# Kernel tuning notes

Measured on AMD Instinct MI355X. Metric: run time of the kernel, lower is better.

## Reference

```python
import jax, jax.numpy as jnp
import numpy as np

B, DIN, F, H, C = 8192, 2048, 2048, 2048, 345
EPS = 1e-5


def setup_inputs() -> dict:
    key = jax.random.key(0)
    ks = jax.random.split(key, 8)
    rng = np.random.default_rng(0)
    # labels and sort order (torch.sort is stable here via argsort kind='stable')
    y_np = rng.integers(0, C, size=B).astype(np.int64)
    order_np = np.argsort(y_np, kind='stable')
    ys = y_np[order_np]
    # per-class random permutations within each sorted segment (torch.randperm per interval)
    shuf1 = np.empty(B, dtype=np.int64)
    shuf2 = np.empty(B, dtype=np.int64)
    for c in np.unique(ys):
        idx = np.nonzero(ys == c)[0]
        shuf1[idx] = rng.permutation(idx)
        shuf2[idx] = rng.permutation(idx)
    s = 0.02  # weight init scale
    return {
        'x': jax.random.normal(ks[0], (B, DIN), jnp.float32),
        'lam': jnp.array([float(rng.beta(0.5, 0.5))], jnp.float32),
        'Wf': jax.random.normal(ks[1], (DIN, F), jnp.float32) * s,
        'bf': jnp.zeros((F,), jnp.float32),
        'W1': jax.random.normal(ks[2], (F, H), jnp.float32) * s,
        'b1': jnp.zeros((H,), jnp.float32),
        'g1': jnp.ones((H,), jnp.float32),
        'be1': jnp.zeros((H,), jnp.float32),
        'W2': jax.random.normal(ks[3], (H, H), jnp.float32) * s,
        'b2': jnp.zeros((H,), jnp.float32),
        'g2': jnp.ones((H,), jnp.float32),
        'be2': jnp.zeros((H,), jnp.float32),
        'W3': jax.random.normal(ks[4], (H, F), jnp.float32) * s,
        'b3': jnp.zeros((F,), jnp.float32),
        'g3': jnp.ones((F,), jnp.float32),
        'be3': jnp.zeros((F,), jnp.float32),
        'Wc': jax.random.normal(ks[5], (F, C), jnp.float32) * s,
        'bc': jnp.zeros((C,), jnp.float32),
        'y': jnp.asarray(y_np),
        'order': jnp.asarray(order_np),
        'shuf1': jnp.asarray(shuf1),
        'shuf2': jnp.asarray(shuf2),
    }


def _bn(x, g, b):
    # BatchNorm1d, training mode: biased batch stats
    m = jnp.mean(x, axis=0)
    v = jnp.var(x, axis=0)
    return (x - m) * jax.lax.rsqrt(v + EPS) * g + b


def reference(x, lam, Wf, bf, W1, b1, g1, be1, W2, b2, g2, be2, W3, b3, g3, be3, Wc, bc, y, order, shuf1, shuf2):
    lam = lam[0]
    xs = x[order]           # sorted-by-label gather (vectorized)
    ys = y[order]
    feat = jax.nn.relu(xs @ Wf + bf)                      # featurizer
    h = jax.nn.relu(_bn(feat @ W1 + b1, g1, be1))         # cdpl projector
    h = jax.nn.relu(_bn(h @ W2 + b2, g2, be2))
    proj = _bn(h @ W3 + b3, g3, be3)
    out = feat @ Wc + bc                                  # classifier logits
    out2, feat2 = out[shuf1], proj[shuf1]                 # per-class shuffles
    out3, feat3 = out[shuf2], proj[shuf2]
    out3 = lam * out2 + (1.0 - lam) * out3
    feat3 = lam * feat2 + (1.0 - lam) * feat3
    mse = lambda a, b: jnp.mean((a - b) ** 2)
    L_ind_logit = mse(out, out2)
    L_hdl_logit = mse(out, out3)
    L_ind_feat = 0.3 * mse(proj, feat2)
    L_hdl_feat = 0.3 * mse(proj, feat3)
    logp = jax.nn.log_softmax(out, axis=-1)
    cl_loss = -jnp.mean(jnp.take_along_axis(logp, ys[:, None], axis=-1))
    C_scale = jax.lax.stop_gradient(jnp.minimum(cl_loss, 1.0))  # .item() -> constant
    loss = cl_loss + C_scale * (lam * (L_ind_logit + L_ind_feat) + (1.0 - lam) * (L_hdl_logit + L_hdl_feat))
    return loss
```

## Files before the change

kernel.cpp:

```cpp
#include <hip/hip_runtime.h>

#define NB   8192
#define NF   2048
#define NC   345
#define NCP  384
#define EPSV 1e-5f

#define SX   (5.75f / 127.0f)
#define SW   (0.115f / 127.0f)
#define SF   (5.2f / 127.0f)
#define SH   (5.75f / 127.0f)
#define ST1  (3.34f / 127.0f)
#define ST2  (3.68f / 127.0f)
#define QX   (1.0f / SX)
#define QW   (1.0f / SW)
#define QF   (1.0f / SF)
#define QH   (1.0f / SH)
#define QT1  (1.0f / ST1)
#define QT2  (1.0f / ST2)

typedef __bf16 bf16x8 __attribute__((ext_vector_type(8)));
typedef float  f32x4  __attribute__((ext_vector_type(4)));
typedef int    i32x4  __attribute__((ext_vector_type(4)));

__device__ __forceinline__ float bs2f(unsigned int u) { return __uint_as_float(u << 16); }
__device__ __forceinline__ unsigned short f2bs(float f) {
    unsigned int u = __float_as_uint(f);
    u += 0x7fffu + ((u >> 16) & 1u);
    return (unsigned short)(u >> 16);
}
__device__ __forceinline__ int q8i(float v, float iq) {
    int t = __float2int_rn(v * iq);
    return t > 127 ? 127 : (t < -127 ? -127 : t);
}

#define GLD16(g, l)                                                                     \
    __builtin_amdgcn_global_load_lds((const __attribute__((address_space(1))) void*)(g),\
                                     (__attribute__((address_space(3))) void*)(l),      \
                                     16, 0, 0)

__global__ void k_gather(const float* __restrict__ x, const int* __restrict__ order,
                         char* __restrict__ xq) {
    const int row = blockIdx.x;
    const long src = order[row];
    const float4* xr = (const float4*)(x + src * 2048);
    float4 a = xr[threadIdx.x * 2 + 0];
    float4 b = xr[threadIdx.x * 2 + 1];
    unsigned int lo = (unsigned)(q8i(a.x, QX) & 255) | ((unsigned)(q8i(a.y, QX) & 255) << 8) |
                      ((unsigned)(q8i(a.z, QX) & 255) << 16) | ((unsigned)(q8i(a.w, QX) & 255) << 24);
    unsigned int hi = (unsigned)(q8i(b.x, QX) & 255) | ((unsigned)(q8i(b.y, QX) & 255) << 8) |
                      ((unsigned)(q8i(b.z, QX) & 255) << 16) | ((unsigned)(q8i(b.w, QX) & 255) << 24);
    uint2 o; o.x = lo; o.y = hi;
    ((uint2*)(xq + (long)row * 2048))[threadIdx.x] = o;
}

__global__ __launch_bounds__(256) void k_transpose4(
        const float* __restrict__ W0, const float* __restrict__ W1,
        const float* __restrict__ W2, const float* __restrict__ W3,
        char* __restrict__ Wt) {
    __shared__ float tile[32][133];
    const float* Wz = (blockIdx.z == 0) ? W0 : (blockIdx.z == 1) ? W1
                     : (blockIdx.z == 2) ? W2 : W3;
    char* out = Wt + (size_t)blockIdx.z * 2048 * 2048;
    const int n0 = blockIdx.x * 32, k0 = blockIdx.y * 128;
    const int t = threadIdx.x;
    #pragma unroll
    for (int i = 0; i < 16; i++) {
        const int e = t + i * 256;
        const int k = e >> 5, n = e & 31;
        tile[n][k] = Wz[(long)(k0 + k) * 2048 + n0 + n];
    }
    __syncthreads();
    #pragma unroll
    for (int i = 0; i < 4; i++) {
        const int e = t + i * 256;
        const int n = e >> 5;
        const int j = (e & 31) * 4;
        unsigned int o = (unsigned)(q8i(tile[n][j + 0], QW) & 255)
                       | ((unsigned)(q8i(tile[n][j + 1], QW) & 255) << 8)
                       | ((unsigned)(q8i(tile[n][j + 2], QW) & 255) << 16)
                       | ((unsigned)(q8i(tile[n][j + 3], QW) & 255) << 24);
        *(unsigned int*)&out[(long)(n0 + n) * 2048 + k0 + j] = o;
    }
}

__global__ void k_transposeC(const float* __restrict__ W, char* __restrict__ Wt8,
                             const float* __restrict__ bc, float* __restrict__ bcp,
                             int K, int N, int Npad) {
    __shared__ float tile[32][33];
    const int n0 = blockIdx.x * 32, k0 = blockIdx.y * 32;
    const int tx = threadIdx.x, ty = threadIdx.y;
    if (blockIdx.x == 0 && blockIdx.y == 0) {
        const int idx = ty * 32 + tx;
        for (int i = idx; i < Npad; i += 256) bcp[i] = (i < N) ? bc[i] : 0.f;
    }
    #pragma unroll
    for (int i = 0; i < 32; i += 8) {
        int n = n0 + tx, k = k0 + ty + i;
        tile[ty + i][tx] = (n < N) ? W[(long)k * N + n] : 0.f;
    }
    __syncthreads();
    #pragma unroll
    for (int i = 0; i < 32; i += 8) {
        int n = n0 + ty + i, k = k0 + tx;
        if (n < Npad) Wt8[(long)n * K + k] = (char)q8i(tile[tx][ty + i], QW);
    }
}

#define BARX  do { asm volatile("" ::: "memory"); __builtin_amdgcn_s_barrier(); \
                   asm volatile("" ::: "memory"); } while (0)
#define LGKM0 asm volatile("s_waitcnt lgkmcnt(0)" ::: "memory")
#define VMW4  asm volatile("s_waitcnt vmcnt(4)" ::: "memory")
#define VMW0  asm volatile("s_waitcnt vmcnt(0)" ::: "memory")

#define RDX(u, AV, BV) do {                                                            \
    const char* A_ = &L[((u) & 3) * 32768];                                            \
    const char* B_ = A_ + 16384;                                                       \
    _Pragma("unroll") for (int m_ = 0; m_ < 8; m_++)                                   \
        AV[m_] = *(const i32x4*)&A_[(wm * 128 + m_ * 16 + frow) * 64 + slt];           \
    _Pragma("unroll") for (int n_ = 0; n_ < 4; n_++)                                   \
        BV[n_] = *(const i32x4*)&B_[(wn * 64 + n_ * 16 + frow) * 64 + slt];            \
} while (0)

#define MMX(AV, BV) do {                                                               \
    __builtin_amdgcn_s_setprio(1);                                                     \
    _Pragma("unroll") for (int n_ = 0; n_ < 4; n_++)                                   \
    _Pragma("unroll") for (int m_ = 0; m_ < 8; m_++)                                   \
        acc[m_][n_] = __builtin_amdgcn_mfma_i32_16x16x64_i8(BV[n_], AV[m_],            \
                                                            acc[m_][n_], 0, 0, 0);    \
    __builtin_amdgcn_s_setprio(0);                                                     \
} while (0)

template <int RELU, int STATS>
__global__ __launch_bounds__(512, 2) void k_gemmq(
    const char* __restrict__ A,
    const char* __restrict__ Bt,
    const float* __restrict__ bias,
    char* __restrict__ C8,
    float* __restrict__ stats,
    float S, float IQ, int N, int K) {
    __shared__ char L[4 * 32768];
    const int tid  = threadIdx.x;
    const int lane = tid & 63;
    const int wv   = tid >> 6;
    const int frow = lane & 15;
    const int kg   = lane >> 4;
    const int wm   = wv >> 2;
    const int wn   = wv & 3;
    const int slt  = (kg ^ ((frow >> 1) & 3)) * 16;

    const int id  = blockIdx.x;
    const int xcd = id & 7, kid = id >> 3;
    const int brow = (xcd * 4 + (kid & 3)) * 256;
    const int bcol = (kid >> 2) * 256;

    const char* pA[2];
    const char* pB[2];
    #pragma unroll
    for (int i = 0; i < 2; i++) {
        const int q = tid + i * 512;
        const int j = q >> 2;
        const int c = (q & 3) ^ ((j >> 1) & 3);
        pA[i] = A  + (long)(brow + j) * K + c * 16;
        pB[i] = Bt + (long)(bcol + j) * K + c * 16;
    }

    i32x4 acc[8][4];
    #pragma unroll
    for (int m = 0; m < 8; m++)
        #pragma unroll
        for (int n = 0; n < 4; n++)
            #pragma unroll
            for (int r = 0; r < 4; r++) acc[m][n][r] = 0;

    auto stage = [&](int s) {
        char* Lb = &L[(s & 3) * 32768];
        const int ko = s * 64;
        GLD16(pA[0] + ko, Lb + wv * 1024);
        GLD16(pA[1] + ko, Lb + 8192 + wv * 1024);
        GLD16(pB[0] + ko, Lb + 16384 + wv * 1024);
        GLD16(pB[1] + ko, Lb + 24576 + wv * 1024);
    };

    i32x4 avA[8], bvA[4], avB[8], bvB[4];

    stage(0); stage(1); stage(2);
    VMW4; BARX;
    RDX(0, avA, bvA);

    for (int i = 0; i < 14; i++) {
        const int t = i * 2;
        RDX(t + 1, avB, bvB); stage(t + 3); MMX(avA, bvA); VMW4; BARX;
        RDX(t + 2, avA, bvA); stage(t + 4); MMX(avB, bvB); VMW4; BARX;
    }
    RDX(29, avB, bvB); stage(31); MMX(avA, bvA); VMW4; BARX;
    RDX(30, avA, bvA); MMX(avB, bvB); VMW0; BARX;
    RDX(31, avB, bvB); MMX(avA, bvA);
    MMX(avB, bvB);

    LGKM0; BARX;
    unsigned short* Ls = (unsigned short*)L;
    const int cbase = bcol + wn * 64 + kg * 4;
    #pragma unroll
    for (int n = 0; n < 4; n++) {
        const int col = cbase + n * 16;
        const float4 bb = *(const float4*)&bias[col];
        float s0_ = 0.f, s1_ = 0.f, s2_ = 0.f, s3_ = 0.f;
        float q0_ = 0.f, q1_ = 0.f, q2_ = 0.f, q3_ = 0.f;
        const int s8 = wn * 16 + n * 4 + kg;
        const int p8 = s8 ^ frow;
        #pragma unroll
        for (int m = 0; m < 8; m++) {
            const int rloc = wm * 128 + m * 16 + frow;
            float v0 = (float)acc[m][n][0] * S + bb.x;
            float v1 = (float)acc[m][n][1] * S + bb.y;
            float v2 = (float)acc[m][n][2] * S + bb.z;
            float v3 = (float)acc[m][n][3] * S + bb.w;
            if (STATS) { s0_ += v0; q0_ += v0 * v0; s1_ += v1; q1_ += v1 * v1;
                         s2_ += v2; q2_ += v2 * v2; s3_ += v3; q3_ += v3 * v3; }
            if (RELU) { v0 = fmaxf(v0, 0.f); v1 = fmaxf(v1, 0.f);
                        v2 = fmaxf(v2, 0.f); v3 = fmaxf(v3, 0.f); }
            ushort4 st; st.x = f2bs(v0); st.y = f2bs(v1); st.z = f2bs(v2); st.w = f2bs(v3);
            *(ushort4*)&Ls[rloc * 256 + p8 * 4] = st;
        }
        if (STATS) {
            #pragma unroll
            for (int off = 1; off <= 8; off <<= 1) {
                s0_ += __shfl_xor(s0_, off); s1_ += __shfl_xor(s1_, off);
                s2_ += __shfl_xor(s2_, off); s3_ += __shfl_xor(s3_, off);
                q0_ += __shfl_xor(q0_, off); q1_ += __shfl_xor(q1_, off);
                q2_ += __shfl_xor(q2_, off); q3_ += __shfl_xor(q3_, off);
            }
            if (frow == 0) {
                atomicAdd(&stats[col + 0], s0_); atomicAdd(&stats[col + 1], s1_);
                atomicAdd(&stats[col + 2], s2_); atomicAdd(&stats[col + 3], s3_);
                atomicAdd(&stats[N + col + 0], q0_); atomicAdd(&stats[N + col + 1], q1_);
                atomicAdd(&stats[N + col + 2], q2_); atomicAdd(&stats[N + col + 3], q3_);
            }
        }
    }
    LGKM0; BARX;
    #pragma unroll
    for (int it = 0; it < 16; it++) {
        const int c  = tid + it * 512;
        const int r  = c >> 5;
        const int a  = c & 31;
        const int x  = r & 15;
        const int a2 = a ^ (x >> 1);
        uint4 v = *(const uint4*)&Ls[r * 256 + a2 * 8];
        if (x & 1) { unsigned tx_ = v.x, ty_ = v.y; v.x = v.z; v.y = v.w; v.z = tx_; v.w = ty_; }
        const long grow = brow + r;
        const int  gcol = bcol + a * 8;
        unsigned int us[8] = {v.x & 0xffffu, v.x >> 16, v.y & 0xffffu, v.y >> 16,
                              v.z & 0xffffu, v.z >> 16, v.w & 0xffffu, v.w >> 16};
        unsigned int b[8];
        #pragma unroll
        for (int j = 0; j < 8; j++) b[j] = (unsigned)(q8i(bs2f(us[j]), IQ) & 255);
        uint2 o;
        o.x = b[0] | (b[1] << 8) | (b[2] << 16) | (b[3] << 24);
        o.y = b[4] | (b[5] << 8) | (b[6] << 16) | (b[7] << 24);
        *(uint2*)&C8[grow * N + gcol] = o;
    }
}

__global__ __launch_bounds__(256) void k_gemmc(const char* __restrict__ A,
                                               const char* __restrict__ Bt,
                                               const float* __restrict__ bias,
                                               unsigned short* __restrict__ outP,
                                               float S, int K) {
    __shared__ char As[2][8192];
    __shared__ char Bs[2][8192];
    const int tid  = threadIdx.x;
    const int lane = tid & 63;
    const int wv   = tid >> 6;
    const int brow = blockIdx.x * 128;
    const int bcol = blockIdx.y * 128;
    const int kz   = blockIdx.z;
    const long k0  = (long)kz * 1024;
    const int wr   = (wv >> 1) * 64;
    const int wc   = (wv & 1) * 64;
    const int frow = lane & 15;
    const int kg   = lane >> 4;
    const int slt  = (kg ^ ((frow >> 1) & 3)) * 16;

    const char* pA[2];
    const char* pB[2];
    #pragma unroll
    for (int i = 0; i < 2; i++) {
        const int q = tid + i * 256;
        const int j = q >> 2;
        const int c = (q & 3) ^ ((j >> 1) & 3);
        pA[i] = A  + (long)(brow + j) * K + k0 + c * 16;
        pB[i] = Bt + (long)(bcol + j) * K + k0 + c * 16;
    }

    i32x4 acc[4][4];
    #pragma unroll
    for (int m = 0; m < 4; m++)
        #pragma unroll
        for (int n = 0; n < 4; n++)
            #pragma unroll
            for (int r = 0; r < 4; r++) acc[m][n][r] = 0;

    auto stage = [&](int t, int b) {
        GLD16(pA[0] + t * 64, As[b] + wv * 1024);
        GLD16(pA[1] + t * 64, As[b] + 4096 + wv * 1024);
        GLD16(pB[0] + t * 64, Bs[b] + wv * 1024);
        GLD16(pB[1] + t * 64, Bs[b] + 4096 + wv * 1024);
    };

    stage(0, 0);
    __syncthreads();
    for (int t = 0; t < 16; t++) {
        if (t < 15) stage(t + 1, (t + 1) & 1);
        const int b = t & 1;
        i32x4 av[4], bv[4];
        #pragma unroll
        for (int m = 0; m < 4; m++)
            av[m] = *(const i32x4*)&As[b][(wr + m * 16 + frow) * 64 + slt];
        #pragma unroll
        for (int n = 0; n < 4; n++)
            bv[n] = *(const i32x4*)&Bs[b][(wc + n * 16 + frow) * 64 + slt];
        #pragma unroll
        for (int m = 0; m < 4; m++)
            #pragma unroll
            for (int n = 0; n < 4; n++)
                acc[m][n] = __builtin_amdgcn_mfma_i32_16x16x64_i8(bv[n], av[m],
                                                                  acc[m][n], 0, 0, 0);
        __syncthreads();
    }
    const int r0 = brow + wr + frow;
    const int c0 = bcol + wc + kg * 4;
    unsigned short* oz = outP + (long)kz * NB * NCP;
    #pragma unroll
    for (int n = 0; n < 4; n++) {
        const int col = c0 + n * 16;
        float4 bb = {0.f, 0.f, 0.f, 0.f};
        if (kz == 0) bb = *(const float4*)&bias[col];
        #pragma unroll
        for (int m = 0; m < 4; m++) {
            const long row = r0 + m * 16;
            ushort4 st;
            st.x = f2bs((float)acc[m][n][0] * S + bb.x);
            st.y = f2bs((float)acc[m][n][1] * S + bb.y);
            st.z = f2bs((float)acc[m][n][2] * S + bb.z);
            st.w = f2bs((float)acc[m][n][3] * S + bb.w);
            *(ushort4*)&oz[row * NCP + col] = st;
        }
    }
}

__global__ void k_bnapplyq8(const char* __restrict__ t8, const float* __restrict__ sums,
                            const float* __restrict__ g, const float* __restrict__ be,
                            char* __restrict__ o8, float St, int ncols) {
    const long i  = ((long)blockIdx.x * blockDim.x + threadIdx.x) * 8;
    const int  c0 = (int)(i & (ncols - 1));
    float sc[8], sh[8];
    #pragma unroll
    for (int j = 0; j < 8; j++) {
        const int c = c0 + j;
        const float m   = sums[c] * (1.f / NB);
        const float var = sums[ncols + c] * (1.f / NB) - m * m;
        const float s   = rsqrtf(var + EPSV) * g[c];
        sc[j] = s * St;
        sh[j] = be[c] - m * s;
    }
    uint2 v = *(const uint2*)(t8 + i);
    unsigned int b[8];
    #pragma unroll
    for (int j = 0; j < 8; j++) {
        const unsigned int w = (j < 4) ? v.x : v.y;
        const int raw = (int)(signed char)((w >> ((j & 3) * 8)) & 0xffu);
        float val = (float)raw * sc[j] + sh[j];
        val = fmaxf(val, 0.f);
        b[j] = (unsigned)(q8i(val, QH) & 255);
    }
    uint2 o;
    o.x = b[0] | (b[1] << 8) | (b[2] << 16) | (b[3] << 24);
    o.y = b[4] | (b[5] << 8) | (b[6] << 16) | (b[7] << 24);
    *(uint2*)(o8 + i) = o;
}

__global__ __launch_bounds__(256) void k_logitloss(const unsigned short* __restrict__ outP,
                            const int* __restrict__ y,
                            const int* __restrict__ order, const int* __restrict__ s1,
                            const int* __restrict__ s2, const float* __restrict__ lamp,
                            float* __restrict__ acc) {
    const int lane = threadIdx.x & 63;
    const int wv   = threadIdx.x >> 6;
    const int wid  = blockIdx.x * 4 + wv;
    const int nw   = gridDim.x * 4;
    const float lam = lamp[0];
    const unsigned short* P1 = outP + (long)NB * NCP;
    float ce = 0.f, d1 = 0.f, d2 = 0.f;
    for (int i = wid; i < NB; i += nw) {
        const long r0 = (long)i * NCP;
        const long r2 = (long)s1[i] * NCP;
        const long r3 = (long)s2[i] * NCP;
        float v[6];
        float mx = -1e30f;
        #pragma unroll
        for (int j = 0; j < 6; j++) {
            const int c = lane + j * 64;
            if (c < NC) {
                const float a  = bs2f(outP[r0 + c]) + bs2f(P1[r0 + c]);
                const float b  = bs2f(outP[r2 + c]) + bs2f(P1[r2 + c]);
                const float cc = bs2f(outP[r3 + c]) + bs2f(P1[r3 + c]);
                const float mix = lam * b + (1.f - lam) * cc;
                v[j] = a;
                d1 += (a - b) * (a - b);
                d2 += (a - mix) * (a - mix);
                mx = fmaxf(mx, a);
            } else v[j] = -1e30f;
        }
        #pragma unroll
        for (int off = 32; off; off >>= 1) mx = fmaxf(mx, __shfl_xor(mx, off));
        float se = 0.f;
        #pragma unroll
        for (int j = 0; j < 6; j++) se += expf(v[j] - mx);
        #pragma unroll
        for (int off = 32; off; off >>= 1) se += __shfl_xor(se, off);
        if (lane == 0) {
            const int yv = y[order[i]];
            const float oy = bs2f(outP[r0 + yv]) + bs2f(P1[r0 + yv]);
            ce += mx + logf(se) - oy;
        }
    }
    #pragma unroll
    for (int off = 32; off; off >>= 1) {
        d1 += __shfl_xor(d1, off);
        d2 += __shfl_xor(d2, off);
    }
    __shared__ float red[4][3];
    if (lane == 0) { red[wv][0] = ce; red[wv][1] = d1; red[wv][2] = d2; }
    __syncthreads();
    if (threadIdx.x == 0) {
        atomicAdd(&acc[0], red[0][0] + red[1][0] + red[2][0] + red[3][0]);
        atomicAdd(&acc[1], red[0][1] + red[1][1] + red[2][1] + red[3][1]);
        atomicAdd(&acc[2], red[0][2] + red[1][2] + red[2][2] + red[3][2]);
    }
}

__global__ __launch_bounds__(256) void k_featloss(const char* __restrict__ t3q,
                           const float* __restrict__ sums,
                           const float* __restrict__ g, const float* __restrict__ be,
                           const int* __restrict__ s1,
                           const int* __restrict__ s2, const float* __restrict__ lamp,
                           float* __restrict__ acc) {
    const int t = threadIdx.x;
    const float lam = lamp[0];
    float sc[8], sh[8];
    #pragma unroll
    for (int j = 0; j < 8; j++) {
        const int c = t * 8 + j;
        const float m   = sums[c] * (1.f / NB);
        const float var = sums[NF + c] * (1.f / NB) - m * m;
        const float s   = rsqrtf(var + EPSV) * g[c];
        sc[j] = s * ST2;
        sh[j] = be[c] - m * s;
    }
    float d1 = 0.f, d2 = 0.f;
    for (int i = blockIdx.x; i < NB; i += gridDim.x) {
        uint2 a = ((const uint2*)(t3q + (long)i * NF))[t];
        uint2 b = ((const uint2*)(t3q + (long)s1[i] * NF))[t];
        uint2 c = ((const uint2*)(t3q + (long)s2[i] * NF))[t];
        #pragma unroll
        for (int j = 0; j < 8; j++) {
            const unsigned int wa = (j < 4) ? a.x : a.y;
            const unsigned int wb = (j < 4) ? b.x : b.y;
            const unsigned int wc_ = (j < 4) ? c.x : c.y;
            const int sh8 = (j & 3) * 8;
            float pa = (float)(int)(signed char)((wa >> sh8) & 0xffu) * sc[j] + sh[j];
            float pb = (float)(int)(signed char)((wb >> sh8) & 0xffu) * sc[j] + sh[j];
            float pc = (float)(int)(signed char)((wc_ >> sh8) & 0xffu) * sc[j] + sh[j];
            float mix = lam * pb + (1.f - lam) * pc;
            d1 += (pa - pb) * (pa - pb);
            d2 += (pa - mix) * (pa - mix);
        }
    }
    #pragma unroll
    for (int off = 32; off; off >>= 1) {
        d1 += __shfl_xor(d1, off);
        d2 += __shfl_xor(d2, off);
    }
    __shared__ float r1[4], r2[4];
    if ((t & 63) == 0) { r1[t >> 6] = d1; r2[t >> 6] = d2; }
    __syncthreads();
    if (t == 0) {
        atomicAdd(&acc[3], r1[0] + r1[1] + r1[2] + r1[3]);
        atomicAdd(&acc[4], r2[0] + r2[1] + r2[2] + r2[3]);
    }
}

__global__ void k_final(const float* __restrict__ acc, const float* __restrict__ lamp,
                        float* __restrict__ outp) {
    const float lam = lamp[0];
    const float cl  = acc[0] * (1.f / NB);
    const float Lil = acc[1] * (1.f / ((float)NB * NC));
    const float Lhl = acc[2] * (1.f / ((float)NB * NC));
    const float Lif = 0.3f * acc[3] * (1.f / ((float)NB * NF));
    const float Lhf = 0.3f * acc[4] * (1.f / ((float)NB * NF));
    const float Cs  = fminf(cl, 1.f);
    outp[0] = cl + Cs * (lam * (Lil + Lif) + (1.f - lam) * (Lhl + Lhf));
}

extern "C" void kernel_launch(void* const* d_in, const int* in_sizes, int n_in,
                              void* d_out, int out_size, void* d_ws, size_t ws_size,
                              hipStream_t stream) {
    const float* x   = (const float*)d_in[0];
    const float* lam = (const float*)d_in[1];
    const float* Wf  = (const float*)d_in[2];
    const float* bf_ = (const float*)d_in[3];
    const float* W1  = (const float*)d_in[4];
    const float* b1  = (const float*)d_in[5];
    const float* g1  = (const float*)d_in[6];
    const float* be1 = (const float*)d_in[7];
    const float* W2  = (const float*)d_in[8];
    const float* b2  = (const float*)d_in[9];
    const float* g2  = (const float*)d_in[10];
    const float* be2 = (const float*)d_in[11];
    const float* W3  = (const float*)d_in[12];
    const float* b3  = (const float*)d_in[13];
    const float* g3  = (const float*)d_in[14];
    const float* be3 = (const float*)d_in[15];
    const float* Wc  = (const float*)d_in[16];
    const float* bc  = (const float*)d_in[17];
    const int* y     = (const int*)d_in[18];
    const int* order = (const int*)d_in[19];
    const int* s1    = (const int*)d_in[20];
    const int* s2    = (const int*)d_in[21];
    float* outp = (float*)d_out;

    char* ws = (char*)d_ws;
    const size_t MB = 1024 * 1024;
    char*  R0  = ws;
    char*  R2  = ws + 16 * MB;
    char*  R3  = ws + 32 * MB;
    unsigned short* outP = (unsigned short*)(ws + 48 * MB);
    char*  WT  = ws + 72 * MB;
    char*  WCT8 = ws + 88 * MB;
    float* stats = (float*)(ws + 89 * MB);
    float* accs  = stats + 3 * 4096;
    float* bcp   = accs + 16;

    hipMemsetAsync(stats, 0, (3 * 4096 + 8) * sizeof(float), stream);

    k_transpose4<<<dim3(64, 16, 4), 256, 0, stream>>>(Wf, W1, W2, W3, WT);
    k_transposeC<<<dim3(12, 64), dim3(32, 8), 0, stream>>>(Wc, WCT8, bc, bcp, 2048, NC, NCP);

    k_gather<<<NB, 256, 0, stream>>>(x, order, R0);

    k_gemmq<1, 0><<<256, 512, 0, stream>>>(R0, WT, bf_, R2, nullptr,
                                           SX * SW, QF, 2048, 2048);
    k_gemmc<<<dim3(64, 3, 2), 256, 0, stream>>>(R2, WCT8, bcp, outP, SF * SW, 2048);
    k_gemmq<0, 1><<<256, 512, 0, stream>>>(R2, WT + 4 * MB, b1, R3, stats,
                                           SF * SW, QT1, 2048, 2048);
    k_bnapplyq8<<<8192, 256, 0, stream>>>(R3, stats, g1, be1, R0, ST1, 2048);
    k_gemmq<0, 1><<<256, 512, 0, stream>>>(R0, WT + 8 * MB, b2, R3, stats + 4096,
                                           SH * SW, QT2, 2048, 2048);
    k_bnapplyq8<<<8192, 256, 0, stream>>>(R3, stats + 4096, g2, be2, R2, ST2, 2048);
    k_gemmq<0, 1><<<256, 512, 0, stream>>>(R2, WT + 12 * MB, b3, R3, stats + 8192,
                                           SH * SW, QT2, 2048, 2048);

    k_logitloss<<<512, 256, 0, stream>>>(outP, y, order, s1, s2, lam, accs);
    k_featloss<<<512, 256, 0, stream>>>(R3, stats + 8192, g3, be3, s1, s2, lam, accs);
    k_final<<<1, 1, 0, stream>>>(accs, lam, outp);
}
```

Baseline: 299.9 us.

## Merge independent kernels into combined launches to cut launch overhead

Three prep kernels (weight transposes, Wc transpose, input gather) become one launch whose work is chosen by block index. The classifier GEMM is moved later and co-launched with the first BN-apply, and the two loss kernels become one launch. The aim is fewer launches and more overlap of small independent work. The cost is mixed block types in one grid, which can change occupancy and scheduling. The classifier GEMM now also runs after the first projector GEMM instead of before it.

```diff
diff --git a/kernel.cpp b/kernel.cpp
--- a/kernel.cpp
+++ b/kernel.cpp
@@ -39,71 +39,70 @@
                                      (__attribute__((address_space(3))) void*)(l),      \
                                      16, 0, 0)
 
-__global__ void k_gather(const float* __restrict__ x, const int* __restrict__ order,
-                         char* __restrict__ xq) {
-    const int row = blockIdx.x;
-    const long src = order[row];
-    const float4* xr = (const float4*)(x + src * 2048);
-    float4 a = xr[threadIdx.x * 2 + 0];
-    float4 b = xr[threadIdx.x * 2 + 1];
-    unsigned int lo = (unsigned)(q8i(a.x, QX) & 255) | ((unsigned)(q8i(a.y, QX) & 255) << 8) |
-                      ((unsigned)(q8i(a.z, QX) & 255) << 16) | ((unsigned)(q8i(a.w, QX) & 255) << 24);
-    unsigned int hi = (unsigned)(q8i(b.x, QX) & 255) | ((unsigned)(q8i(b.y, QX) & 255) << 8) |
-                      ((unsigned)(q8i(b.z, QX) & 255) << 16) | ((unsigned)(q8i(b.w, QX) & 255) << 24);
-    uint2 o; o.x = lo; o.y = hi;
-    ((uint2*)(xq + (long)row * 2048))[threadIdx.x] = o;
-}
-
-__global__ __launch_bounds__(256) void k_transpose4(
+__global__ __launch_bounds__(256) void k_prep(
         const float* __restrict__ W0, const float* __restrict__ W1,
         const float* __restrict__ W2, const float* __restrict__ W3,
-        char* __restrict__ Wt) {
+        char* __restrict__ Wt,
+        const float* __restrict__ x, const int* __restrict__ order,
+        char* __restrict__ xq,
+        const float* __restrict__ Wc, char* __restrict__ WCT8,
+        const float* __restrict__ bc, float* __restrict__ bcp) {
     __shared__ float tile[32][133];
-    const float* Wz = (blockIdx.z == 0) ? W0 : (blockIdx.z == 1) ? W1
-                     : (blockIdx.z == 2) ? W2 : W3;
-    char* out = Wt + (size_t)blockIdx.z * 2048 * 2048;
-    const int n0 = blockIdx.x * 32, k0 = blockIdx.y * 128;
+    const int blk = blockIdx.x;
     const int t = threadIdx.x;
-    #pragma unroll
-    for (int i = 0; i < 16; i++) {
-        const int e = t + i * 256;
-        const int k = e >> 5, n = e & 31;
-        tile[n][k] = Wz[(long)(k0 + k) * 2048 + n0 + n];
-    }
-    __syncthreads();
-    #pragma unroll
-    for (int i = 0; i < 4; i++) {
-        const int e = t + i * 256;
-        const int n = e >> 5;
-        const int j = (e & 31) * 4;
-        unsigned int o = (unsigned)(q8i(tile[n][j + 0], QW) & 255)
-                       | ((unsigned)(q8i(tile[n][j + 1], QW) & 255) << 8)
-                       | ((unsigned)(q8i(tile[n][j + 2], QW) & 255) << 16)
-                       | ((unsigned)(q8i(tile[n][j + 3], QW) & 255) << 24);
-        *(unsigned int*)&out[(long)(n0 + n) * 2048 + k0 + j] = o;
-    }
-}
-
-__global__ void k_transposeC(const float* __restrict__ W, char* __restrict__ Wt8,
-                             const float* __restrict__ bc, float* __restrict__ bcp,
-                             int K, int N, int Npad) {
-    __shared__ float tile[32][33];
-    const int n0 = blockIdx.x * 32, k0 = blockIdx.y * 32;
-    const int tx = threadIdx.x, ty = threadIdx.y;
-    if (blockIdx.x == 0 && blockIdx.y == 0) {
-        const int idx = ty * 32 + tx;
-        for (int i = idx; i < Npad; i += 256) bcp[i] = (i < N) ? bc[i] : 0.f;
-    }
-    #pragma unroll
-    for (int i = 0; i < 32; i += 8) {
-        int n = n0 + tx, k = k0 + ty + i;
-        tile[ty + i][tx] = (n < N) ? W[(long)k * N + n] : 0.f;
-    }
-    __syncthreads();
-    #pragma unroll
-    for (int i = 0; i < 32; i += 8) {
-        int n = n0 + ty + i, k = k0 + tx;
-        if (n < Npad) Wt8[(long)n * K + k] = (char)q8i(tile[tx][ty + i], QW);
+    if (blk < 4096) {
+        const int bz = blk >> 10, by = (blk >> 6) & 15, bx = blk & 63;
+        const float* Wz = (bz == 0) ? W0 : (bz == 1) ? W1 : (bz == 2) ? W2 : W3;
+        char* out = Wt + (size_t)bz * 2048 * 2048;
+        const int n0 = bx * 32, k0 = by * 128;
+        #pragma unroll
+        for (int i = 0; i < 16; i++) {
+            const int e = t + i * 256;
+            const int k = e >> 5, n = e & 31;
+            tile[n][k] = Wz[(long)(k0 + k) * 2048 + n0 + n];
+        }
+        __syncthreads();
+        #pragma unroll
+        for (int i = 0; i < 4; i++) {
+            const int e = t + i * 256;
+            const int n = e >> 5;
+            const int j = (e & 31) * 4;
+            unsigned int o = (unsigned)(q8i(tile[n][j + 0], QW) & 255)
+                           | ((unsigned)(q8i(tile[n][j + 1], QW) & 255) << 8)
+                           | ((unsigned)(q8i(tile[n][j + 2], QW) & 255) << 16)
+                           | ((unsigned)(q8i(tile[n][j + 3], QW) & 255) << 24);
+            *(unsigned int*)&out[(long)(n0 + n) * 2048 + k0 + j] = o;
+        }
+    } else if (blk < 12288) {
+        const int row = blk - 4096;
+        const long src = order[row];
+        const float4* xr = (const float4*)(x + src * 2048);
+        float4 a = xr[t * 2 + 0];
+        float4 b = xr[t * 2 + 1];
+        unsigned int lo = (unsigned)(q8i(a.x, QX) & 255) | ((unsigned)(q8i(a.y, QX) & 255) << 8) |
+                          ((unsigned)(q8i(a.z, QX) & 255) << 16) | ((unsigned)(q8i(a.w, QX) & 255) << 24);
+        unsigned int hi = (unsigned)(q8i(b.x, QX) & 255) | ((unsigned)(q8i(b.y, QX) & 255) << 8) |
+                          ((unsigned)(q8i(b.z, QX) & 255) << 16) | ((unsigned)(q8i(b.w, QX) & 255) << 24);
+        uint2 o; o.x = lo; o.y = hi;
+        ((uint2*)(xq + (long)row * 2048))[t] = o;
+    } else {
+        const int idx = blk - 12288;
+        const int bx = idx % 12, by = idx / 12;
+        const int tx = t & 31, ty = t >> 5;
+        const int n0 = bx * 32, k0 = by * 32;
+        if (idx == 0)
+            for (int i = t; i < NCP; i += 256) bcp[i] = (i < NC) ? bc[i] : 0.f;
+        #pragma unroll
+        for (int i = 0; i < 32; i += 8) {
+            int n = n0 + tx, k = k0 + ty + i;
+            tile[ty + i][tx] = (n < NC) ? Wc[(long)k * NC + n] : 0.f;
+        }
+        __syncthreads();
+        #pragma unroll
+        for (int i = 0; i < 32; i += 8) {
+            int n = n0 + ty + i, k = k0 + tx;
+            if (n < NCP) WCT8[(long)n * 2048 + k] = (char)q8i(tile[tx][ty + i], QW);
+        }
     }
 }
 
@@ -263,90 +262,124 @@
     }
 }
 
-__global__ __launch_bounds__(256) void k_gemmc(const char* __restrict__ A,
-                                               const char* __restrict__ Bt,
-                                               const float* __restrict__ bias,
-                                               unsigned short* __restrict__ outP,
-                                               float S, int K) {
+__global__ __launch_bounds__(256) void k_gemmc_bn(
+        const char* __restrict__ A, const char* __restrict__ Bt,
+        const float* __restrict__ bias, unsigned short* __restrict__ outP, float S,
+        const char* __restrict__ t8, const float* __restrict__ sums,
+        const float* __restrict__ g, const float* __restrict__ be,
+        char* __restrict__ o8, float St) {
     __shared__ char As[2][8192];
     __shared__ char Bs[2][8192];
-    const int tid  = threadIdx.x;
-    const int lane = tid & 63;
-    const int wv   = tid >> 6;
-    const int brow = blockIdx.x * 128;
-    const int bcol = blockIdx.y * 128;
-    const int kz   = blockIdx.z;
-    const long k0  = (long)kz * 1024;
-    const int wr   = (wv >> 1) * 64;
-    const int wc   = (wv & 1) * 64;
-    const int frow = lane & 15;
-    const int kg   = lane >> 4;
-    const int slt  = (kg ^ ((frow >> 1) & 3)) * 16;
-
-    const char* pA[2];
-    const char* pB[2];
-    #pragma unroll
-    for (int i = 0; i < 2; i++) {
-        const int q = tid + i * 256;
-        const int j = q >> 2;
-        const int c = (q & 3) ^ ((j >> 1) & 3);
-        pA[i] = A  + (long)(brow + j) * K + k0 + c * 16;
-        pB[i] = Bt + (long)(bcol + j) * K + k0 + c * 16;
-    }
-
-    i32x4 acc[4][4];
-    #pragma unroll
-    for (int m = 0; m < 4; m++)
-        #pragma unroll
-        for (int n = 0; n < 4; n++)
-            #pragma unroll
-            for (int r = 0; r < 4; r++) acc[m][n][r] = 0;
-
-    auto stage = [&](int t, int b) {
-        GLD16(pA[0] + t * 64, As[b] + wv * 1024);
-        GLD16(pA[1] + t * 64, As[b] + 4096 + wv * 1024);
-        GLD16(pB[0] + t * 64, Bs[b] + wv * 1024);
-        GLD16(pB[1] + t * 64, Bs[b] + 4096 + wv * 1024);
-    };
-
-    stage(0, 0);
-    __syncthreads();
-    for (int t = 0; t < 16; t++) {
-        if (t < 15) stage(t + 1, (t + 1) & 1);
-        const int b = t & 1;
-        i32x4 av[4], bv[4];
+    const int tid = threadIdx.x;
+    if (blockIdx.x < 384) {
+        const int id   = blockIdx.x;
+        const int bx   = id & 63, r_ = id >> 6;
+        const int by   = r_ % 3,  kz = r_ / 3;
+        const int lane = tid & 63;
+        const int wv   = tid >> 6;
+        const int brow = bx * 128;
+        const int bcol = by * 128;
+        const long k0  = (long)kz * 1024;
+        const int wr   = (wv >> 1) * 64;
+        const int wc   = (wv & 1) * 64;
+        const int frow = lane & 15;
+        const int kg   = lane >> 4;
+        const int slt  = (kg ^ ((frow >> 1) & 3)) * 16;
+        const int K    = 2048;
+
+        const char* pA[2];
+        const char* pB[2];
+        #pragma unroll
+        for (int i = 0; i < 2; i++) {
+            const int q = tid + i * 256;
+            const int j = q >> 2;
+            const int c = (q & 3) ^ ((j >> 1) & 3);
+            pA[i] = A  + (long)(brow + j) * K + k0 + c * 16;
+            pB[i] = Bt + (long)(bcol + j) * K + k0 + c * 16;
+        }
+
+        i32x4 acc[4][4];
         #pragma unroll
         for (int m = 0; m < 4; m++)
-            av[m] = *(const i32x4*)&As[b][(wr + m * 16 + frow) * 64 + slt];
-        #pragma unroll
-        for (int n = 0; n < 4; n++)
-            bv[n] = *(const i32x4*)&Bs[b][(wc + n * 16 + frow) * 64 + slt];
-        #pragma unroll
-        for (int m = 0; m < 4; m++)
             #pragma unroll
             for (int n = 0; n < 4; n++)
-                acc[m][n] = __builtin_amdgcn_mfma_i32_16x16x64_i8(bv[n], av[m],
-                                                                  acc[m][n], 0, 0, 0);
+                #pragma unroll
+                for (int r = 0; r < 4; r++) acc[m][n][r] = 0;
+
+        auto stage = [&](int t, int b) {
+            GLD16(pA[0] + t * 64, As[b] + wv * 1024);
+            GLD16(pA[1] + t * 64, As[b] + 4096 + wv * 1024);
+            GLD16(pB[0] + t * 64, Bs[b] + wv * 1024);
+            GLD16(pB[1] + t * 64, Bs[b] + 4096 + wv * 1024);
+        };
+
+        stage(0, 0);
         __syncthreads();
-    }
-    const int r0 = brow + wr + frow;
-    const int c0 = bcol + wc + kg * 4;
-    unsigned short* oz = outP + (long)kz * NB * NCP;
-    #pragma unroll
-    for (int n = 0; n < 4; n++) {
-        const int col = c0 + n * 16;
-        float4 bb = {0.f, 0.f, 0.f, 0.f};
-        if (kz == 0) bb = *(const float4*)&bias[col];
-        #pragma unroll
-        for (int m = 0; m < 4; m++) {
-            const long row = r0 + m * 16;
-            ushort4 st;
-            st.x = f2bs((float)acc[m][n][0] * S + bb.x);
-            st.y = f2bs((float)acc[m][n][1] * S + bb.y);
-            st.z = f2bs((float)acc[m][n][2] * S + bb.z);
-            st.w = f2bs((float)acc[m][n][3] * S + bb.w);
-            *(ushort4*)&oz[row * NCP + col] = st;
-        }
+        for (int t = 0; t < 16; t++) {
+            if (t < 15) stage(t + 1, (t + 1) & 1);
+            const int b = t & 1;
+            i32x4 av[4], bv[4];
+            #pragma unroll
+            for (int m = 0; m < 4; m++)
+                av[m] = *(const i32x4*)&As[b][(wr + m * 16 + frow) * 64 + slt];
+            #pragma unroll
+            for (int n = 0; n < 4; n++)
+                bv[n] = *(const i32x4*)&Bs[b][(wc + n * 16 + frow) * 64 + slt];
+            #pragma unroll
+            for (int m = 0; m < 4; m++)
+                #pragma unroll
+                for (int n = 0; n < 4; n++)
+                    acc[m][n] = __builtin_amdgcn_mfma_i32_16x16x64_i8(bv[n], av[m],
+                                                                      acc[m][n], 0, 0, 0);
+            __syncthreads();
+        }
+        const int r0 = brow + wr + frow;
+        const int c0 = bcol + wc + kg * 4;
+        unsigned short* oz = outP + (long)kz * NB * NCP;
+        #pragma unroll
+        for (int n = 0; n < 4; n++) {
+            const int col = c0 + n * 16;
+            float4 bb = {0.f, 0.f, 0.f, 0.f};
+            if (kz == 0) bb = *(const float4*)&bias[col];
+            #pragma unroll
+            for (int m = 0; m < 4; m++) {
+                const long row = r0 + m * 16;
+                ushort4 st;
+                st.x = f2bs((float)acc[m][n][0] * S + bb.x);
+                st.y = f2bs((float)acc[m][n][1] * S + bb.y);
+                st.z = f2bs((float)acc[m][n][2] * S + bb.z);
+                st.w = f2bs((float)acc[m][n][3] * S + bb.w);
+                *(ushort4*)&oz[row * NCP + col] = st;
+            }
+        }
+    } else {
+        const long bid = blockIdx.x - 384;
+        const long i  = (bid * 256 + tid) * 8;
+        const int  c0 = (int)(i & (NF - 1));
+        float sc[8], sh[8];
+        #pragma unroll
+        for (int j = 0; j < 8; j++) {
+            const int c = c0 + j;
+            const float m   = sums[c] * (1.f / NB);
+            const float var = sums[NF + c] * (1.f / NB) - m * m;
+            const float s   = rsqrtf(var + EPSV) * g[c];
+            sc[j] = s * St;
+            sh[j] = be[c] - m * s;
+        }
+        uint2 v = *(const uint2*)(t8 + i);
+        unsigned int b[8];
+        #pragma unroll
+        for (int j = 0; j < 8; j++) {
+            const unsigned int w = (j < 4) ? v.x : v.y;
+            const int raw = (int)(signed char)((w >> ((j & 3) * 8)) & 0xffu);
+            float val = (float)raw * sc[j] + sh[j];
+            val = fmaxf(val, 0.f);
+            b[j] = (unsigned)(q8i(val, QH) & 255);
+        }
+        uint2 o;
+        o.x = b[0] | (b[1] << 8) | (b[2] << 16) | (b[3] << 24);
+        o.y = b[4] | (b[5] << 8) | (b[6] << 16) | (b[7] << 24);
+        *(uint2*)(o8 + i) = o;
     }
 }
 
@@ -381,114 +414,109 @@
     *(uint2*)(o8 + i) = o;
 }
 
-__global__ __launch_bounds__(256) void k_logitloss(const unsigned short* __restrict__ outP,
-                            const int* __restrict__ y,
-                            const int* __restrict__ order, const int* __restrict__ s1,
-                            const int* __restrict__ s2, const float* __restrict__ lamp,
-                            float* __restrict__ acc) {
-    const int lane = threadIdx.x & 63;
-    const int wv   = threadIdx.x >> 6;
-    const int wid  = blockIdx.x * 4 + wv;
-    const int nw   = gridDim.x * 4;
+__global__ __launch_bounds__(256) void k_loss(
+        const unsigned short* __restrict__ outP,
+        const int* __restrict__ y, const int* __restrict__ order,
+        const int* __restrict__ s1, const int* __restrict__ s2,
+        const float* __restrict__ lamp, float* __restrict__ acc,
+        const char* __restrict__ t3q, const float* __restrict__ sums,
+        const float* __restrict__ g, const float* __restrict__ be) {
+    __shared__ float red[4][3];
     const float lam = lamp[0];
-    const unsigned short* P1 = outP + (long)NB * NCP;
-    float ce = 0.f, d1 = 0.f, d2 = 0.f;
-    for (int i = wid; i < NB; i += nw) {
-        const long r0 = (long)i * NCP;
-        const long r2 = (long)s1[i] * NCP;
-        const long r3 = (long)s2[i] * NCP;
-        float v[6];
-        float mx = -1e30f;
-        #pragma unroll
-        for (int j = 0; j < 6; j++) {
-            const int c = lane + j * 64;
-            if (c < NC) {
-                const float a  = bs2f(outP[r0 + c]) + bs2f(P1[r0 + c]);
-                const float b  = bs2f(outP[r2 + c]) + bs2f(P1[r2 + c]);
-                const float cc = bs2f(outP[r3 + c]) + bs2f(P1[r3 + c]);
-                const float mix = lam * b + (1.f - lam) * cc;
-                v[j] = a;
-                d1 += (a - b) * (a - b);
-                d2 += (a - mix) * (a - mix);
-                mx = fmaxf(mx, a);
-            } else v[j] = -1e30f;
-        }
-        #pragma unroll
-        for (int off = 32; off; off >>= 1) mx = fmaxf(mx, __shfl_xor(mx, off));
-        float se = 0.f;
-        #pragma unroll
-        for (int j = 0; j < 6; j++) se += expf(v[j] - mx);
-        #pragma unroll
-        for (int off = 32; off; off >>= 1) se += __shfl_xor(se, off);
-        if (lane == 0) {
-            const int yv = y[order[i]];
-            const float oy = bs2f(outP[r0 + yv]) + bs2f(P1[r0 + yv]);
-            ce += mx + logf(se) - oy;
-        }
-    }
-    #pragma unroll
-    for (int off = 32; off; off >>= 1) {
-        d1 += __shfl_xor(d1, off);
-        d2 += __shfl_xor(d2, off);
-    }
-    __shared__ float red[4][3];
-    if (lane == 0) { red[wv][0] = ce; red[wv][1] = d1; red[wv][2] = d2; }
-    __syncthreads();
-    if (threadIdx.x == 0) {
-        atomicAdd(&acc[0], red[0][0] + red[1][0] + red[2][0] + red[3][0]);
-        atomicAdd(&acc[1], red[0][1] + red[1][1] + red[2][1] + red[3][1]);
-        atomicAdd(&acc[2], red[0][2] + red[1][2] + red[2][2] + red[3][2]);
-    }
-}
-
-__global__ __launch_bounds__(256) void k_featloss(const char* __restrict__ t3q,
-                           const float* __restrict__ sums,
-                           const float* __restrict__ g, const float* __restrict__ be,
-                           const int* __restrict__ s1,
-                           const int* __restrict__ s2, const float* __restrict__ lamp,
-                           float* __restrict__ acc) {
-    const int t = threadIdx.x;
-    const float lam = lamp[0];
-    float sc[8], sh[8];
-    #pragma unroll
-    for (int j = 0; j < 8; j++) {
-        const int c = t * 8 + j;
-        const float m   = sums[c] * (1.f / NB);
-        const float var = sums[NF + c] * (1.f / NB) - m * m;
-        const float s   = rsqrtf(var + EPSV) * g[c];
-        sc[j] = s * ST2;
-        sh[j] = be[c] - m * s;
-    }
-    float d1 = 0.f, d2 = 0.f;
-    for (int i = blockIdx.x; i < NB; i += gridDim.x) {
-        uint2 a = ((const uint2*)(t3q + (long)i * NF))[t];
-        uint2 b = ((const uint2*)(t3q + (long)s1[i] * NF))[t];
-        uint2 c = ((const uint2*)(t3q + (long)s2[i] * NF))[t];
+    if (blockIdx.x < 512) {
+        const int lane = threadIdx.x & 63;
+        const int wv   = threadIdx.x >> 6;
+        const int wid  = blockIdx.x * 4 + wv;
+        const int nw   = 512 * 4;
+        const unsigned short* P1 = outP + (long)NB * NCP;
+        float ce = 0.f, d1 = 0.f, d2 = 0.f;
+        for (int i = wid; i < NB; i += nw) {
+            const long r0 = (long)i * NCP;
+            const long r2 = (long)s1[i] * NCP;
+            const long r3 = (long)s2[i] * NCP;
+            float v[6];
+            float mx = -1e30f;
+            #pragma unroll
+            for (int j = 0; j < 6; j++) {
+                const int c = lane + j * 64;
+                if (c < NC) {
+                    const float a  = bs2f(outP[r0 + c]) + bs2f(P1[r0 + c]);
+                    const float b  = bs2f(outP[r2 + c]) + bs2f(P1[r2 + c]);
+                    const float cc = bs2f(outP[r3 + c]) + bs2f(P1[r3 + c]);
+                    const float mix = lam * b + (1.f - lam) * cc;
+                    v[j] = a;
+                    d1 += (a - b) * (a - b);
+                    d2 += (a - mix) * (a - mix);
+                    mx = fmaxf(mx, a);
+                } else v[j] = -1e30f;
+            }
+            #pragma unroll
+            for (int off = 32; off; off >>= 1) mx = fmaxf(mx, __shfl_xor(mx, off));
+            float se = 0.f;
+            #pragma unroll
+            for (int j = 0; j < 6; j++) se += expf(v[j] - mx);
+            #pragma unroll
+            for (int off = 32; off; off >>= 1) se += __shfl_xor(se, off);
+            if (lane == 0) {
+                const int yv = y[order[i]];
+                const float oy = bs2f(outP[r0 + yv]) + bs2f(P1[r0 + yv]);
+                ce += mx + logf(se) - oy;
+            }
+        }
+        #pragma unroll
+        for (int off = 32; off; off >>= 1) {
+            d1 += __shfl_xor(d1, off);
+            d2 += __shfl_xor(d2, off);
+        }
+        if (lane == 0) { red[wv][0] = ce; red[wv][1] = d1; red[wv][2] = d2; }
+        __syncthreads();
+        if (threadIdx.x == 0) {
+            atomicAdd(&acc[0], red[0][0] + red[1][0] + red[2][0] + red[3][0]);
+            atomicAdd(&acc[1], red[0][1] + red[1][1] + red[2][1] + red[3][1]);
+            atomicAdd(&acc[2], red[0][2] + red[1][2] + red[2][2] + red[3][2]);
+        }
+    } else {
+        const int t = threadIdx.x;
+        float sc[8], sh[8];
         #pragma unroll
         for (int j = 0; j < 8; j++) {
-            const unsigned int wa = (j < 4) ? a.x : a.y;
-            const unsigned int wb = (j < 4) ? b.x : b.y;
-            const unsigned int wc_ = (j < 4) ? c.x : c.y;
-            const int sh8 = (j & 3) * 8;
-            float pa = (float)(int)(signed char)((wa >> sh8) & 0xffu) * sc[j] + sh[j];
-            float pb = (float)(int)(signed char)((wb >> sh8) & 0xffu) * sc[j] + sh[j];
-            float pc = (float)(int)(signed char)((wc_ >> sh8) & 0xffu) * sc[j] + sh[j];
-            float mix = lam * pb + (1.f - lam) * pc;
-            d1 += (pa - pb) * (pa - pb);
-            d2 += (pa - mix) * (pa - mix);
-        }
-    }
-    #pragma unroll
-    for (int off = 32; off; off >>= 1) {
-        d1 += __shfl_xor(d1, off);
-        d2 += __shfl_xor(d2, off);
-    }
-    __shared__ float r1[4], r2[4];
-    if ((t & 63) == 0) { r1[t >> 6] = d1; r2[t >> 6] = d2; }
-    __syncthreads();
-    if (t == 0) {
-        atomicAdd(&acc[3], r1[0] + r1[1] + r1[2] + r1[3]);
-        atomicAdd(&acc[4], r2[0] + r2[1] + r2[2] + r2[3]);
+            const int c = t * 8 + j;
+            const float m   = sums[c] * (1.f / NB);
+            const float var = sums[NF + c] * (1.f / NB) - m * m;
+            const float s   = rsqrtf(var + EPSV) * g[c];
+            sc[j] = s * ST2;
+            sh[j] = be[c] - m * s;
+        }
+        float d1 = 0.f, d2 = 0.f;
+        for (int i = blockIdx.x - 512; i < NB; i += 512) {
+            uint2 a = ((const uint2*)(t3q + (long)i * NF))[t];
+            uint2 b = ((const uint2*)(t3q + (long)s1[i] * NF))[t];
+            uint2 c = ((const uint2*)(t3q + (long)s2[i] * NF))[t];
+            #pragma unroll
+            for (int j = 0; j < 8; j++) {
+                const unsigned int wa = (j < 4) ? a.x : a.y;
+                const unsigned int wb = (j < 4) ? b.x : b.y;
+                const unsigned int wc_ = (j < 4) ? c.x : c.y;
+                const int sh8 = (j & 3) * 8;
+                float pa = (float)(int)(signed char)((wa >> sh8) & 0xffu) * sc[j] + sh[j];
+                float pb = (float)(int)(signed char)((wb >> sh8) & 0xffu) * sc[j] + sh[j];
+                float pc = (float)(int)(signed char)((wc_ >> sh8) & 0xffu) * sc[j] + sh[j];
+                float mix = lam * pb + (1.f - lam) * pc;
+                d1 += (pa - pb) * (pa - pb);
+                d2 += (pa - mix) * (pa - mix);
+            }
+        }
+        #pragma unroll
+        for (int off = 32; off; off >>= 1) {
+            d1 += __shfl_xor(d1, off);
+            d2 += __shfl_xor(d2, off);
+        }
+        if ((t & 63) == 0) { red[t >> 6][0] = d1; red[t >> 6][1] = d2; }
+        __syncthreads();
+        if (t == 0) {
+            atomicAdd(&acc[3], red[0][0] + red[1][0] + red[2][0] + red[3][0]);
+            atomicAdd(&acc[4], red[0][1] + red[1][1] + red[2][1] + red[3][1]);
+        }
     }
 }
 
@@ -545,24 +573,22 @@
 
     hipMemsetAsync(stats, 0, (3 * 4096 + 8) * sizeof(float), stream);
 
-    k_transpose4<<<dim3(64, 16, 4), 256, 0, stream>>>(Wf, W1, W2, W3, WT);
-    k_transposeC<<<dim3(12, 64), dim3(32, 8), 0, stream>>>(Wc, WCT8, bc, bcp, 2048, NC, NCP);
-
-    k_gather<<<NB, 256, 0, stream>>>(x, order, R0);
+    k_prep<<<13056, 256, 0, stream>>>(Wf, W1, W2, W3, WT, x, order, R0,
+                                      Wc, WCT8, bc, bcp);
 
     k_gemmq<1, 0><<<256, 512, 0, stream>>>(R0, WT, bf_, R2, nullptr,
                                            SX * SW, QF, 2048, 2048);
-    k_gemmc<<<dim3(64, 3, 2), 256, 0, stream>>>(R2, WCT8, bcp, outP, SF * SW, 2048);
     k_gemmq<0, 1><<<256, 512, 0, stream>>>(R2, WT + 4 * MB, b1, R3, stats,
                                            SF * SW, QT1, 2048, 2048);
-    k_bnapplyq8<<<8192, 256, 0, stream>>>(R3, stats, g1, be1, R0, ST1, 2048);
+    k_gemmc_bn<<<384 + 8192, 256, 0, stream>>>(R2, WCT8, bcp, outP, SF * SW,
+                                               R3, stats, g1, be1, R0, ST1);
     k_gemmq<0, 1><<<256, 512, 0, stream>>>(R0, WT + 8 * MB, b2, R3, stats + 4096,
                                            SH * SW, QT2, 2048, 2048);
     k_bnapplyq8<<<8192, 256, 0, stream>>>(R3, stats + 4096, g2, be2, R2, ST2, 2048);
     k_gemmq<0, 1><<<256, 512, 0, stream>>>(R2, WT + 12 * MB, b3, R3, stats + 8192,
                                            SH * SW, QT2, 2048, 2048);
 
-    k_logitloss<<<512, 256, 0, stream>>>(outP, y, order, s1, s2, lam, accs);
-    k_featloss<<<512, 256, 0, stream>>>(R3, stats + 8192, g3, be3, s1, s2, lam, accs);
+    k_loss<<<1024, 256, 0, stream>>>(outP, y, order, s1, s2, lam, accs,
+                                     R3, stats + 8192, g3, be3);
     k_final<<<1, 1, 0, stream>>>(accs, lam, outp);
 }
```

Result: faster. 282.0 us (-5.9%).
